# Kernel optimization log

Hardware: AMD Instinct MI355X
Metric: run time of the kernel (lower is better)

The kernel has to match this reference:

```python
import jax, jax.numpy as jnp
import numpy as np

N_NODES = 50000
N_EDGES = 800000
IN_CH, HID_CH, OUT_CH = 100, 128, 47
ORIG_SIZE = 25000


def sage_conv(x, edge_index, w_l, b_l, w_r):
    """PyG-style SAGEConv with mean aggregation.
    out = lin_l(mean_{j in N(i)} x_j) + lin_r(x_i)
    edge_index[0]=source, edge_index[1]=target.
    """
    src, dst = edge_index[0], edge_index[1]
    n = x.shape[0]
    # gather source features, scatter-sum into targets  [N, d]
    agg = jax.ops.segment_sum(x[src], dst, num_segments=n)
    deg = jax.ops.segment_sum(jnp.ones((src.shape[0],), x.dtype), dst, num_segments=n)
    mean = agg / jnp.maximum(deg, 1.0)[:, None]
    return mean @ w_l + b_l + x @ w_r


def setup_inputs() -> dict:
    key = jax.random.key(0)
    ks = jax.random.split(key, 8)
    x = jax.random.normal(ks[0], (N_NODES, IN_CH), dtype=jnp.float32)
    edge_index = jax.random.randint(ks[1], (2, N_EDGES), 0, N_NODES, dtype=jnp.int32)
    s1 = 1.0 / np.sqrt(IN_CH)
    s2 = 1.0 / np.sqrt(HID_CH)
    w1_l = jax.random.uniform(ks[2], (IN_CH, HID_CH), jnp.float32, -s1, s1)
    b1_l = jax.random.uniform(ks[3], (HID_CH,), jnp.float32, -s1, s1)
    w1_r = jax.random.uniform(ks[4], (IN_CH, HID_CH), jnp.float32, -s1, s1)
    w2_l = jax.random.uniform(ks[5], (HID_CH, OUT_CH), jnp.float32, -s2, s2)
    b2_l = jax.random.uniform(ks[6], (OUT_CH,), jnp.float32, -s2, s2)
    w2_r = jax.random.uniform(ks[7], (HID_CH, OUT_CH), jnp.float32, -s2, s2)
    return {"x": x, "edge_index": edge_index, "original_size": ORIG_SIZE,
            "w1_l": w1_l, "b1_l": b1_l, "w1_r": w1_r,
            "w2_l": w2_l, "b2_l": b2_l, "w2_r": w2_r}


def reference(x, edge_index, original_size, w1_l, b1_l, w1_r, w2_l, b2_l, w2_r):
    h = sage_conv(x, edge_index, w1_l, b1_l, w1_r)   # [N, hidden]
    h = sage_conv(h, edge_index, w2_l, b2_l, w2_r)   # [N, out]
    logp = jax.nn.log_softmax(h, axis=1)
    return logp[:original_size]
```

## Files before the change

### kernel.cpp

```cpp
#include <hip/hip_runtime.h>
#include <hip/hip_fp16.h>
#include <math.h>

constexpr int N    = 50000;
constexpr int E    = 800000;
constexpr int CIN  = 100;
constexpr int CH   = 128;
constexpr int COUT = 47;
constexpr int NOUT = 25000;
constexpr int CP   = 48;
constexpr int TN   = 128;
constexpr int NT   = (N + TN - 1) / TN;

constexpr int HS  = 136;
constexpr int W1K = 256;
constexpr int W2K = 128;
constexpr int A1S = 256;

constexpr int NBUK = (N + 255) / 256;
constexpr int ECH  = 2048;
constexpr int NCH  = (E + ECH - 1) / ECH;

constexpr int CB = (N * 32) / 256;
constexpr int PB = 193;

typedef float f32x4 __attribute__((ext_vector_type(4)));
typedef short v8s  __attribute__((ext_vector_type(8)));

__device__ __forceinline__ void bsplit(float f, ushort& h, ushort& l) {
    uint u = __float_as_uint(f);
    h = (ushort)(u >> 16);
    float fh = __uint_as_float(u & 0xffff0000u);
    l = (ushort)(__float_as_uint(f - fh) >> 16);
}

__device__ __forceinline__ void unpack8(uint4 v, v8s& ah, v8s& al) {
    union { uint4 u; __half2 h[4]; } V; V.u = v;
    ushort hh[8], ll[8];
    #pragma unroll
    for (int p = 0; p < 4; ++p) {
        float2 f = __half22float2(V.h[p]);
        bsplit(f.x, hh[2 * p],     ll[2 * p]);
        bsplit(f.y, hh[2 * p + 1], ll[2 * p + 1]);
    }
    ah = v8s{(short)hh[0], (short)hh[1], (short)hh[2], (short)hh[3],
             (short)hh[4], (short)hh[5], (short)hh[6], (short)hh[7]};
    al = v8s{(short)ll[0], (short)ll[1], (short)ll[2], (short)ll[3],
             (short)ll[4], (short)ll[5], (short)ll[6], (short)ll[7]};
}

__global__ __launch_bounds__(256) void pre_kernel(
        const int* __restrict__ dst, int* __restrict__ lhist,
        const float* __restrict__ x, __half* __restrict__ x16,
        __half* __restrict__ a1x,
        const float* __restrict__ w1l, const float* __restrict__ w1r,
        const float* __restrict__ w2l, const float* __restrict__ w2r,
        const float* __restrict__ b2l,
        ushort* __restrict__ w1T, ushort* __restrict__ w2T,
        float* __restrict__ b2cat) {
    __shared__ int h[NBUK];
    int bid = blockIdx.x, t = threadIdx.x;
    if (bid < NCH) {
        for (int i = t; i < NBUK; i += 256) h[i] = 0;
        __syncthreads();
        int e0 = bid * ECH + t * 8;
        if (e0 < E) {
            int4 d0 = *(const int4*)(dst + e0);
            int4 d1 = *(const int4*)(dst + e0 + 4);
            int dd[8] = {d0.x, d0.y, d0.z, d0.w, d1.x, d1.y, d1.z, d1.w};
            #pragma unroll
            for (int k = 0; k < 8; ++k) atomicAdd(&h[dd[k] >> 8], 1);
        }
        __syncthreads();
        for (int i = t; i < NBUK; i += 256) lhist[bid * NBUK + i] = h[i];
    } else if (bid < NCH + CB) {
        int j = (bid - NCH) * 256 + t;
        int row = j >> 5, s = j & 31;
        uint2 u = make_uint2(0u, 0u);
        if (s < 25) {
            float4 v = ((const float4*)x)[row * 25 + s];
            __half2 h0 = __floats2half2_rn(v.x, v.y);
            __half2 h1 = __floats2half2_rn(v.z, v.w);
            union { __half2 h[2]; uint2 u; } U;
            U.h[0] = h0; U.h[1] = h1;
            u = U.u;
            ((uint2*)x16)[row * 25 + s] = u;
        }
        ((uint2*)a1x)[(size_t)row * 64 + 32 + s] = u;
    } else {
        int i = (bid - NCH - CB) * 256 + t;
        if (i < 128 * W1K) {
            int n = i >> 8, k = i & 255;
            float v = 0.0f;
            if (k < 100)                    v = w1l[(size_t)k * CH + n];
            else if (k >= 128 && k < 228)   v = w1r[(size_t)(k - 128) * CH + n];
            ushort hh, ll; bsplit(v, hh, ll);
            w1T[i] = hh; w1T[128 * W1K + i] = ll;
        } else if (i < 128 * W1K + 128 * W2K) {
            int j2 = i - 128 * W1K;
            int n = j2 >> 7, k = j2 & 127;
            float v = 0.0f;
            if (n < COUT)                      v = w2l[(size_t)k * COUT + n];
            else if (n >= 64 && n < 64 + COUT) v = w2r[(size_t)k * COUT + (n - 64)];
            ushort hh, ll; bsplit(v, hh, ll);
            w2T[j2] = hh; w2T[128 * W2K + j2] = ll;
        } else {
            int j2 = i - (128 * W1K + 128 * W2K);
            if (j2 < 128) b2cat[j2] = (j2 >= 64 && j2 < 64 + COUT) ? b2l[j2 - 64] : 0.0f;
        }
    }
}

__global__ __launch_bounds__(256) void scan_buckets(int* __restrict__ lhist,
        int* __restrict__ tot) {
    __shared__ int s[256];
    int b = blockIdx.x, t = threadIdx.x;
    int carry = 0;
    for (int c0 = 0; c0 < NCH; c0 += 256) {
        int c = c0 + t;
        int v = (c < NCH) ? lhist[(size_t)c * NBUK + b] : 0;
        s[t] = v;
        __syncthreads();
        for (int off = 1; off < 256; off <<= 1) {
            int a = s[t];
            int u = (t >= off) ? s[t - off] : 0;
            __syncthreads();
            s[t] = a + u;
            __syncthreads();
        }
        if (c < NCH) lhist[(size_t)c * NBUK + b] = carry + s[t] - v;
        carry += s[255];
        __syncthreads();
    }
    if (t == 0) tot[b] = carry;
}

__global__ __launch_bounds__(256) void scan_base(const int* __restrict__ tot,
        int* __restrict__ base) {
    __shared__ int s[256];
    int t = threadIdx.x;
    int v = (t < NBUK) ? tot[t] : 0;
    s[t] = v;
    __syncthreads();
    for (int off = 1; off < 256; off <<= 1) {
        int a = s[t];
        int u = (t >= off) ? s[t - off] : 0;
        __syncthreads();
        s[t] = a + u;
        __syncthreads();
    }
    if (t < NBUK) base[t] = s[t] - v;
    if (t == 0) base[NBUK] = s[255];
}

__global__ __launch_bounds__(256) void scatter_coarse(const int* __restrict__ src,
        const int* __restrict__ dst, const int* __restrict__ lhist,
        const int* __restrict__ base, int* __restrict__ ebuf) {
    __shared__ int cur[NBUK];
    int c = blockIdx.x, t = threadIdx.x;
    for (int i = t; i < NBUK; i += 256) cur[i] = base[i] + lhist[(size_t)c * NBUK + i];
    __syncthreads();
    int e0 = c * ECH + t * 8;
    if (e0 < E) {
        int4 d0 = *(const int4*)(dst + e0);
        int4 d1 = *(const int4*)(dst + e0 + 4);
        int4 s0 = *(const int4*)(src + e0);
        int4 s1 = *(const int4*)(src + e0 + 4);
        int dd[8] = {d0.x, d0.y, d0.z, d0.w, d1.x, d1.y, d1.z, d1.w};
        int ss[8] = {s0.x, s0.y, s0.z, s0.w, s1.x, s1.y, s1.z, s1.w};
        #pragma unroll
        for (int k = 0; k < 8; ++k) {
            int p = atomicAdd(&cur[dd[k] >> 8], 1);
            ebuf[p] = (ss[k] << 8) | (dd[k] & 255);
        }
    }
}

__global__ __launch_bounds__(256) void build_csr(const int* __restrict__ ebuf,
        const int* __restrict__ base, int* __restrict__ row_ptr,
        int* __restrict__ col) {
    __shared__ int cntL[256];
    __shared__ int s[256];
    int b = blockIdx.x, t = threadIdx.x;
    int segS = base[b], segE = base[b + 1];
    cntL[t] = 0;
    __syncthreads();
    for (int i = segS + t; i < segE; i += 256)
        atomicAdd(&cntL[ebuf[i] & 255], 1);
    __syncthreads();
    int v = cntL[t];
    s[t] = v;
    __syncthreads();
    for (int off = 1; off < 256; off <<= 1) {
        int a = s[t];
        int u = (t >= off) ? s[t - off] : 0;
        __syncthreads();
        s[t] = a + u;
        __syncthreads();
    }
    int start = segS + s[t] - v;
    int node = b * 256 + t;
    if (node < N) row_ptr[node] = start;
    if (b == NBUK - 1 && t == 0) row_ptr[N] = E;
    cntL[t] = start;
    __syncthreads();
    for (int i = segS + t; i < segE; i += 256) {
        int v2 = ebuf[i];
        int p = atomicAdd(&cntL[v2 & 255], 1);
        col[p] = v2 >> 8;
    }
}

__global__ __launch_bounds__(256) void gather1_kernel(const __half* __restrict__ x16,
        const int* __restrict__ row_ptr, const int* __restrict__ col,
        __half* __restrict__ a1x) {
    int t = threadIdx.x;
    int n = blockIdx.x * 4 + (t >> 6);
    int l = t & 63, half = l >> 5, li = l & 31;
    int b = row_ptr[n], e = row_ptr[n + 1];
    float inv = 1.0f / (float)max(e - b, 1);
    const uint2* xb = (const uint2*)x16;
    bool act = li < 25;
    float4 s0 = make_float4(0.f, 0.f, 0.f, 0.f);
    float4 s1 = make_float4(0.f, 0.f, 0.f, 0.f);
    float4 s2 = make_float4(0.f, 0.f, 0.f, 0.f);
    float4 s3 = make_float4(0.f, 0.f, 0.f, 0.f);
    union { uint2 u; __half2 h[2]; } U0, U1, U2, U3;
    int j = b + half;
    for (; j + 6 < e; j += 8) {
        int c0 = col[j], c1 = col[j + 2], c2 = col[j + 4], c3 = col[j + 6];
        if (act) {
            U0.u = xb[(size_t)c0 * 25 + li];
            U1.u = xb[(size_t)c1 * 25 + li];
            U2.u = xb[(size_t)c2 * 25 + li];
            U3.u = xb[(size_t)c3 * 25 + li];
            float2 f0a = __half22float2(U0.h[0]), f0b = __half22float2(U0.h[1]);
            float2 f1a = __half22float2(U1.h[0]), f1b = __half22float2(U1.h[1]);
            float2 f2a = __half22float2(U2.h[0]), f2b = __half22float2(U2.h[1]);
            float2 f3a = __half22float2(U3.h[0]), f3b = __half22float2(U3.h[1]);
            s0.x += f0a.x; s0.y += f0a.y; s0.z += f0b.x; s0.w += f0b.y;
            s1.x += f1a.x; s1.y += f1a.y; s1.z += f1b.x; s1.w += f1b.y;
            s2.x += f2a.x; s2.y += f2a.y; s2.z += f2b.x; s2.w += f2b.y;
            s3.x += f3a.x; s3.y += f3a.y; s3.z += f3b.x; s3.w += f3b.y;
        }
    }
    for (; j < e; j += 2) {
        int c0 = col[j];
        if (act) {
            U0.u = xb[(size_t)c0 * 25 + li];
            float2 f0a = __half22float2(U0.h[0]), f0b = __half22float2(U0.h[1]);
            s0.x += f0a.x; s0.y += f0a.y; s0.z += f0b.x; s0.w += f0b.y;
        }
    }
    float4 s = make_float4(s0.x + s1.x + s2.x + s3.x,
                           s0.y + s1.y + s2.y + s3.y,
                           s0.z + s1.z + s2.z + s3.z,
                           s0.w + s1.w + s2.w + s3.w);
    s.x += __shfl_xor(s.x, 32, 64);
    s.y += __shfl_xor(s.y, 32, 64);
    s.z += __shfl_xor(s.z, 32, 64);
    s.w += __shfl_xor(s.w, 32, 64);
    if (half == 0) {
        __half2 p0 = __floats2half2_rn(s.x * inv, s.y * inv);
        __half2 p1 = __floats2half2_rn(s.z * inv, s.w * inv);
        union { __half2 h[2]; uint2 u; } P;
        P.h[0] = p0; P.h[1] = p1;
        ((uint2*)a1x)[(size_t)n * 64 + li] = P.u;
    }
}

__global__ __launch_bounds__(256) void fused_gemm(
        const __half* __restrict__ a1x,
        const ushort* __restrict__ w1T, const float* __restrict__ b1l,
        const ushort* __restrict__ w2T, const float* __restrict__ b2cat,
        __half* __restrict__ gsrc16, float* __restrict__ gself) {
    __shared__ __align__(16) uint lds_u[17408];
    ushort* Hh = (ushort*)lds_u;
    ushort* Hl = Hh + 128 * HS;

    int t = threadIdx.x;
    int lane = t & 63;
    int wv = __builtin_amdgcn_readfirstlane(t >> 6);
    int nh = wv & 1, chh = wv >> 1;
    int l15 = lane & 15, lg = lane >> 4;
    int base = blockIdx.x * TN;

    const ushort* w1Th = w1T;
    const ushort* w1Tl = w1T + 128 * W1K;
    const ushort* w2Th = w2T;
    const ushort* w2Tl = w2T + 128 * W2K;

    f32x4 acc[4][4];
    #pragma unroll
    for (int nt = 0; nt < 4; ++nt) {
        float bv = b1l[chh * 64 + nt * 16 + l15];
        #pragma unroll
        for (int mt = 0; mt < 4; ++mt)
            acc[mt][nt] = f32x4{bv, bv, bv, bv};
    }

    #pragma unroll 2
    for (int ks = 0; ks < 8; ++ks) {
        int k0 = ks * 32 + lg * 8;
        v8s ahf[4], alf[4];
        #pragma unroll
        for (int mt = 0; mt < 4; ++mt) {
            int row = base + nh * 64 + mt * 16 + l15;
            int rr = row < N ? row : N - 1;
            uint4 v = *(const uint4*)(a1x + (size_t)rr * A1S + k0);
            unpack8(v, ahf[mt], alf[mt]);
        }
        #pragma unroll
        for (int nt = 0; nt < 4; ++nt) {
            int n = chh * 64 + nt * 16 + l15;
            v8s bhf = *(const v8s*)(w1Th + (size_t)n * W1K + k0);
            v8s blf = *(const v8s*)(w1Tl + (size_t)n * W1K + k0);
            #pragma unroll
            for (int mt = 0; mt < 4; ++mt) {
                acc[mt][nt] = __builtin_amdgcn_mfma_f32_16x16x32_bf16(
                    ahf[mt], bhf, acc[mt][nt], 0, 0, 0);
                acc[mt][nt] = __builtin_amdgcn_mfma_f32_16x16x32_bf16(
                    alf[mt], bhf, acc[mt][nt], 0, 0, 0);
                acc[mt][nt] = __builtin_amdgcn_mfma_f32_16x16x32_bf16(
                    ahf[mt], blf, acc[mt][nt], 0, 0, 0);
            }
        }
    }

    #pragma unroll
    for (int mt = 0; mt < 4; ++mt) {
        #pragma unroll
        for (int nt = 0; nt < 4; ++nt) {
            int ch = chh * 64 + nt * 16 + l15;
            #pragma unroll
            for (int r = 0; r < 4; ++r) {
                int node = nh * 64 + mt * 16 + lg * 4 + r;
                ushort h, l; bsplit(acc[mt][nt][r], h, l);
                Hh[node * HS + ch] = h;
                Hl[node * HS + ch] = l;
            }
        }
    }
    __syncthreads();

    bool skip = (chh == 1) && (base >= NOUT);
    if (!skip) {
        #pragma unroll
        for (int nt = 0; nt < 4; ++nt) {
            float bv = b2cat[chh * 64 + nt * 16 + l15];
            #pragma unroll
            for (int mt = 0; mt < 4; ++mt)
                acc[mt][nt] = f32x4{bv, bv, bv, bv};
        }
        #pragma unroll
        for (int ks = 0; ks < 4; ++ks) {
            v8s ahf[4], alf[4];
            #pragma unroll
            for (int mt = 0; mt < 4; ++mt) {
                int node = nh * 64 + mt * 16 + l15;
                int ko = ks * 32 + lg * 8;
                ahf[mt] = *(const v8s*)(Hh + node * HS + ko);
                alf[mt] = *(const v8s*)(Hl + node * HS + ko);
            }
            int kg = ks * 32 + lg * 8;
            #pragma unroll
            for (int nt = 0; nt < 4; ++nt) {
                int n = chh * 64 + nt * 16 + l15;
                v8s bhf = *(const v8s*)(w2Th + (size_t)n * W2K + kg);
                v8s blf = *(const v8s*)(w2Tl + (size_t)n * W2K + kg);
                #pragma unroll
                for (int mt = 0; mt < 4; ++mt) {
                    acc[mt][nt] = __builtin_amdgcn_mfma_f32_16x16x32_bf16(
                        ahf[mt], bhf, acc[mt][nt], 0, 0, 0);
                    acc[mt][nt] = __builtin_amdgcn_mfma_f32_16x16x32_bf16(
                        alf[mt], bhf, acc[mt][nt], 0, 0, 0);
                    acc[mt][nt] = __builtin_amdgcn_mfma_f32_16x16x32_bf16(
                        ahf[mt], blf, acc[mt][nt], 0, 0, 0);
                }
            }
        }
        int lim = chh ? NOUT : N;
        #pragma unroll
        for (int nt = 0; nt < 3; ++nt) {
            int colc = nt * 16 + l15;
            #pragma unroll
            for (int mt = 0; mt < 4; ++mt) {
                #pragma unroll
                for (int r = 0; r < 4; ++r) {
                    int node = base + nh * 64 + mt * 16 + lg * 4 + r;
                    if (node < lim) {
                        if (chh) gself[(size_t)node * CP + colc] = acc[mt][nt][r];
                        else gsrc16[(size_t)node * CP + colc] =
                                 __float2half(acc[mt][nt][r]);
                    }
                }
            }
        }
    }
}

__global__ __launch_bounds__(256) void final_kernel(const __half* __restrict__ gsrc16,
        const float* __restrict__ gself, const int* __restrict__ row_ptr,
        const int* __restrict__ col, float* __restrict__ out) {
    int t = threadIdx.x;
    int n = blockIdx.x * 4 + (t >> 6);
    int c = t & 63;
    int b = row_ptr[n], e = row_ptr[n + 1];
    float inv = 1.0f / (float)max(e - b, 1);
    float a0 = 0.f, a1 = 0.f, a2 = 0.f, a3 = 0.f;
    if (c < CP) {
        int j = b;
        for (; j + 3 < e; j += 4) {
            a0 += __half2float(gsrc16[(size_t)col[j]     * CP + c]);
            a1 += __half2float(gsrc16[(size_t)col[j + 1] * CP + c]);
            a2 += __half2float(gsrc16[(size_t)col[j + 2] * CP + c]);
            a3 += __half2float(gsrc16[(size_t)col[j + 3] * CP + c]);
        }
        for (; j < e; ++j) a0 += __half2float(gsrc16[(size_t)col[j] * CP + c]);
    }
    float val = (c < COUT)
        ? (((a0 + a1) + (a2 + a3)) * inv + gself[(size_t)n * CP + c]) : -INFINITY;
    float m = val;
    #pragma unroll
    for (int off = 32; off > 0; off >>= 1) m = fmaxf(m, __shfl_xor(m, off, 64));
    float ex = (c < COUT) ? expf(val - m) : 0.f;
    float ssum = ex;
    #pragma unroll
    for (int off = 32; off > 0; off >>= 1) ssum += __shfl_xor(ssum, off, 64);
    if (c < COUT)
        __builtin_nontemporal_store(val - m - logf(ssum),
                                    out + (size_t)n * COUT + c);
}

extern "C" void kernel_launch(void* const* d_in, const int* in_sizes, int n_in,
                              void* d_out, int out_size, void* d_ws, size_t ws_size,
                              hipStream_t stream) {
    const float* x   = (const float*)d_in[0];
    const int*   ei  = (const int*)d_in[1];
    const int*   src = ei;
    const int*   dst = ei + E;
    const float* w1l = (const float*)d_in[3];
    const float* b1l = (const float*)d_in[4];
    const float* w1r = (const float*)d_in[5];
    const float* w2l = (const float*)d_in[6];
    const float* b2l = (const float*)d_in[7];
    const float* w2r = (const float*)d_in[8];
    float* out = (float*)d_out;

    int* row_ptr = (int*)d_ws;
    int* lhist   = row_ptr + N + 1;
    int* tot     = lhist + (size_t)NCH * NBUK;
    int* base    = tot + NBUK;
    int* ebuf    = base + NBUK + 1;
    int* col     = ebuf + E;
    size_t intWords = (size_t)(N + 1) + (size_t)NCH * NBUK + NBUK + (NBUK + 1)
                      + E + E;
    intWords = (intWords + 3) & ~(size_t)3;
    float* gself  = (float*)d_ws + intWords;
    float* b2cat  = gself + (size_t)NOUT * CP;
    __half* gsrc16 = (__half*)(b2cat + 128);
    __half* x16    = gsrc16 + (size_t)N * CP;
    __half* a1x    = x16 + (size_t)N * CIN;
    ushort* w1T   = (ushort*)(a1x + (size_t)N * A1S);
    ushort* w2T   = w1T + 2 * 128 * W1K;

    pre_kernel    <<<NCH + CB + PB, 256, 0, stream>>>(dst, lhist, x, x16, a1x,
                                                      w1l, w1r, w2l, w2r, b2l,
                                                      w1T, w2T, b2cat);
    scan_buckets  <<<NBUK, 256, 0, stream>>>(lhist, tot);
    scan_base     <<<1, 256, 0, stream>>>(tot, base);
    scatter_coarse<<<NCH, 256, 0, stream>>>(src, dst, lhist, base, ebuf);
    build_csr     <<<NBUK, 256, 0, stream>>>(ebuf, base, row_ptr, col);
    gather1_kernel<<<N / 4, 256, 0, stream>>>(x16, row_ptr, col, a1x);
    fused_gemm    <<<NT, 256, 0, stream>>>(a1x, w1T, b1l, w2T, b2cat,
                                           gsrc16, gself);
    final_kernel  <<<NOUT / 4, 256, 0, stream>>>(gsrc16, gself, row_ptr, col, out);
}
```

Before: 203.4 us.

## Fold base scan into scatter/CSR kernels and store hidden layer as fp16

Removes the single-block scan_base launch by having every scatter_coarse and build_csr block recompute the exclusive prefix over bucket totals in shared memory. The fused GEMM now stores the layer-1 hidden tile as one fp16 array instead of bf16 high/low split pairs, halving LDS use and stores, and unpacks it into the hi/lo bf16 operands (unpack8) for the second GEMM. The cost is redundant per-block scans and reduced precision of the hidden activations (fp16 rounding of h).

Measured after the change: 202.6 us (median of 2 runs). No clear change (-0.4%).

```diff
diff --git a/kernel.cpp b/kernel.cpp
--- a/kernel.cpp
+++ b/kernel.cpp
@@ -135,30 +135,23 @@
     if (t == 0) tot[b] = carry;
 }
 
-__global__ __launch_bounds__(256) void scan_base(const int* __restrict__ tot,
-        int* __restrict__ base) {
-    __shared__ int s[256];
-    int t = threadIdx.x;
-    int v = (t < NBUK) ? tot[t] : 0;
-    s[t] = v;
-    __syncthreads();
-    for (int off = 1; off < 256; off <<= 1) {
-        int a = s[t];
-        int u = (t >= off) ? s[t - off] : 0;
-        __syncthreads();
-        s[t] = a + u;
-        __syncthreads();
-    }
-    if (t < NBUK) base[t] = s[t] - v;
-    if (t == 0) base[NBUK] = s[255];
-}
-
 __global__ __launch_bounds__(256) void scatter_coarse(const int* __restrict__ src,
         const int* __restrict__ dst, const int* __restrict__ lhist,
-        const int* __restrict__ base, int* __restrict__ ebuf) {
+        const int* __restrict__ tot, int* __restrict__ ebuf) {
+    __shared__ int sb[256];
     __shared__ int cur[NBUK];
     int c = blockIdx.x, t = threadIdx.x;
-    for (int i = t; i < NBUK; i += 256) cur[i] = base[i] + lhist[(size_t)c * NBUK + i];
+    int v = (t < NBUK) ? tot[t] : 0;
+    sb[t] = v;
+    __syncthreads();
+    for (int off = 1; off < 256; off <<= 1) {
+        int a = sb[t];
+        int u = (t >= off) ? sb[t - off] : 0;
+        __syncthreads();
+        sb[t] = a + u;
+        __syncthreads();
+    }
+    if (t < NBUK) cur[t] = (sb[t] - v) + lhist[(size_t)c * NBUK + t];
     __syncthreads();
     int e0 = c * ECH + t * 8;
     if (e0 < E) {
@@ -177,12 +170,25 @@
 }
 
 __global__ __launch_bounds__(256) void build_csr(const int* __restrict__ ebuf,
-        const int* __restrict__ base, int* __restrict__ row_ptr,
+        const int* __restrict__ tot, int* __restrict__ row_ptr,
         int* __restrict__ col) {
+    __shared__ int sb[256];
     __shared__ int cntL[256];
     __shared__ int s[256];
     int b = blockIdx.x, t = threadIdx.x;
-    int segS = base[b], segE = base[b + 1];
+    int v0 = (t < NBUK) ? tot[t] : 0;
+    sb[t] = v0;
+    __syncthreads();
+    for (int off = 1; off < 256; off <<= 1) {
+        int a = sb[t];
+        int u = (t >= off) ? sb[t - off] : 0;
+        __syncthreads();
+        sb[t] = a + u;
+        __syncthreads();
+    }
+    int tb = tot[b];
+    int segE = sb[b];
+    int segS = segE - tb;
     cntL[t] = 0;
     __syncthreads();
     for (int i = segS + t; i < segE; i += 256)
@@ -274,9 +280,8 @@
         const ushort* __restrict__ w1T, const float* __restrict__ b1l,
         const ushort* __restrict__ w2T, const float* __restrict__ b2cat,
         __half* __restrict__ gsrc16, float* __restrict__ gself) {
-    __shared__ __align__(16) uint lds_u[17408];
-    ushort* Hh = (ushort*)lds_u;
-    ushort* Hl = Hh + 128 * HS;
+    __shared__ __align__(16) uint lds_u[8704];
+    __half* H16 = (__half*)lds_u;
 
     int t = threadIdx.x;
     int lane = t & 63;
@@ -335,9 +340,7 @@
             #pragma unroll
             for (int r = 0; r < 4; ++r) {
                 int node = nh * 64 + mt * 16 + lg * 4 + r;
-                ushort h, l; bsplit(acc[mt][nt][r], h, l);
-                Hh[node * HS + ch] = h;
-                Hl[node * HS + ch] = l;
+                H16[node * HS + ch] = __float2half(acc[mt][nt][r]);
             }
         }
     }
@@ -359,8 +362,8 @@
             for (int mt = 0; mt < 4; ++mt) {
                 int node = nh * 64 + mt * 16 + l15;
                 int ko = ks * 32 + lg * 8;
-                ahf[mt] = *(const v8s*)(Hh + node * HS + ko);
-                alf[mt] = *(const v8s*)(Hl + node * HS + ko);
+                uint4 v = *(const uint4*)(H16 + node * HS + ko);
+                unpack8(v, ahf[mt], alf[mt]);
             }
             int kg = ks * 32 + lg * 8;
             #pragma unroll
@@ -450,11 +453,9 @@
     int* row_ptr = (int*)d_ws;
     int* lhist   = row_ptr + N + 1;
     int* tot     = lhist + (size_t)NCH * NBUK;
-    int* base    = tot + NBUK;
-    int* ebuf    = base + NBUK + 1;
+    int* ebuf    = tot + NBUK;
     int* col     = ebuf + E;
-    size_t intWords = (size_t)(N + 1) + (size_t)NCH * NBUK + NBUK + (NBUK + 1)
-                      + E + E;
+    size_t intWords = (size_t)(N + 1) + (size_t)NCH * NBUK + NBUK + E + E;
     intWords = (intWords + 3) & ~(size_t)3;
     float* gself  = (float*)d_ws + intWords;
     float* b2cat  = gself + (size_t)NOUT * CP;
@@ -468,9 +469,8 @@
                                                       w1l, w1r, w2l, w2r, b2l,
                                                       w1T, w2T, b2cat);
     scan_buckets  <<<NBUK, 256, 0, stream>>>(lhist, tot);
-    scan_base     <<<1, 256, 0, stream>>>(tot, base);
-    scatter_coarse<<<NCH, 256, 0, stream>>>(src, dst, lhist, base, ebuf);
-    build_csr     <<<NBUK, 256, 0, stream>>>(ebuf, base, row_ptr, col);
+    scatter_coarse<<<NCH, 256, 0, stream>>>(src, dst, lhist, tot, ebuf);
+    build_csr     <<<NBUK, 256, 0, stream>>>(ebuf, tot, row_ptr, col);
     gather1_kernel<<<N / 4, 256, 0, stream>>>(x16, row_ptr, col, a1x);
     fused_gemm    <<<NT, 256, 0, stream>>>(a1x, w1T, b1l, w2T, b2cat,
                                            gsrc16, gself);
```
